# Kernel tuning notes

Measured on AMD Instinct MI355X. Metric: run time of the kernel, lower is better.

Reference implementation:

```python
import jax, jax.numpy as jnp
import numpy as np
import math


def get_slopes(n_heads: int) -> jnp.ndarray:
    """ALiBi head-specific slopes, matching the torch reference."""
    n = 2 ** int(math.floor(math.log2(n_heads)))
    m0 = 2.0 ** (-8.0 / n)
    m = m0 ** jnp.arange(1, n + 1, dtype=jnp.float32)
    if n < n_heads:
        mh0 = 2.0 ** (-4.0 / n)
        mh = mh0 ** jnp.arange(1, 1 + 2 * (n_heads - n), 2, dtype=jnp.float32)
        m = jnp.concatenate([m, mh])
    return m.reshape(1, -1, 1, 1)  # [1, h, 1, 1]


def setup_inputs() -> dict:
    key = jax.random.key(0)
    kq, kk, kv, kb = jax.random.split(key, 4)
    b, h, s_q, s_kv, d = 2, 16, 2048, 2048, 128
    return {
        "query": jax.random.normal(kq, (b, h, s_q, d), dtype=jnp.float32),
        "key": jax.random.normal(kk, (b, h, s_kv, d), dtype=jnp.float32),
        "value": jax.random.normal(kv, (b, h, s_kv, d), dtype=jnp.float32),
        "bias": jax.random.normal(kb, (1, 1, s_q, s_kv), dtype=jnp.float32),
        "is_causal": 1,
        "is_infer": 0,
        "is_alibi": 1,
    }


def reference(query, key, value, bias, is_causal, is_infer, is_alibi):
    _, h, s_q, d = query.shape
    s_kv = key.shape[2]
    attn_scale = 1.0 / math.sqrt(d)

    # S = Q K^T * scale, in fp32 (matches S.to(torch.float32))
    S = jnp.einsum("bhqd,bhkd->bhqk", query, key).astype(jnp.float32) * attn_scale

    if bias is not None:
        S = S + bias

    if is_alibi:
        # relative position (k - q) scaled by per-head slope
        rel = jnp.arange(s_kv, dtype=jnp.float32) - jnp.arange(s_q, dtype=jnp.float32)[:, None]
        S = S + rel * get_slopes(h)

    if is_causal:
        causal_mask = jnp.triu(jnp.ones((s_q, s_kv), dtype=bool), k=1)
        S = jnp.where(causal_mask, -jnp.inf, S)

    Stats = None
    if not is_infer:
        row_max = jnp.max(S, axis=-1, keepdims=True)
        row_sum = jnp.sum(jnp.exp(S - row_max), axis=-1, keepdims=True)
        Stats = row_max + jnp.log(row_sum)  # logsumexp, [b,h,s_q,1]

    P = jax.nn.softmax(S, axis=-1).astype(value.dtype)
    O = jnp.einsum("bhqk,bhkd->bhqd", P, value)
    return (O, Stats)
```

## Files before the change

kernel.cpp:

```cpp
#include <hip/hip_runtime.h>
#include <hip/hip_bf16.h>
#include <math.h>

typedef __bf16 bf16;
typedef __attribute__((ext_vector_type(8))) __bf16 bf16x8;
typedef __attribute__((ext_vector_type(4))) __bf16 bf16x4;
typedef __attribute__((ext_vector_type(4))) float f32x4;
typedef __attribute__((ext_vector_type(16))) float f32x16;
typedef __attribute__((ext_vector_type(4))) unsigned int u32x4;

constexpr int NB = 2, NH = 16, SQ = 2048, SKV = 2048, DH = 128;
constexpr int QB = 128, KVB = 64;
constexpr float SM_SCALE = 0.08838834764831845f;
constexpr float LOG2E = 1.4426950408889634f;
constexpr float DEFER_THR = 7.0f;

#define GLD_LDS(g, l) __builtin_amdgcn_global_load_lds( \
    (const __attribute__((address_space(1))) void*)(g), \
    (__attribute__((address_space(3))) void*)(l), 16, 0, 0)

__device__ __forceinline__ unsigned cvt_pk_bf16(float lo, float hi) {
    unsigned r;
    asm("v_cvt_pk_bf16_f32 %0, %1, %2" : "=v"(r) : "v"(lo), "v"(hi));
    return r;
}
__device__ __forceinline__ void permswap(unsigned &a, unsigned &b) {
    asm("v_permlane32_swap_b32 %0, %1" : "+v"(a), "+v"(b));
}

__global__ __launch_bounds__(256)
void cvt_k_kernel(const float* __restrict__ src, bf16* __restrict__ dst) {
    const size_t i = ((size_t)blockIdx.x * 256 + threadIdx.x) * 8;
    float4 a = *(const float4*)(src + i);
    float4 b = *(const float4*)(src + i + 4);
    bf16x8 f;
    f[0]=(bf16)a.x; f[1]=(bf16)a.y; f[2]=(bf16)a.z; f[3]=(bf16)a.w;
    f[4]=(bf16)b.x; f[5]=(bf16)b.y; f[6]=(bf16)b.z; f[7]=(bf16)b.w;
    *(bf16x8*)(dst + i) = f;
}

__global__ __launch_bounds__(256)
void tr_v_kernel(const float* __restrict__ src, bf16* __restrict__ dst) {
    __shared__ float Tl[64][65];
    const int bh  = blockIdx.y;
    const int kv0 = (int)(blockIdx.x >> 1) * 64;
    const int d0  = (int)(blockIdx.x & 1) * 64;
    const int t   = threadIdx.x;
    const float* sp = src + (size_t)bh * SQ * DH;
#pragma unroll
    for (int i = 0; i < 4; ++i) {
        const int row = i * 16 + (t >> 4);
        const int c4  = (t & 15) * 4;
        *(float4*)&Tl[row][c4] = *(const float4*)(sp + (size_t)(kv0 + row) * DH + d0 + c4);
    }
    __syncthreads();
    bf16* dp = dst + (size_t)bh * DH * SKV;
#pragma unroll
    for (int i = 0; i < 4; ++i) {
        const int d  = i * 16 + (t >> 4);
        const int k4 = (t & 15) * 4;
        bf16x4 o;
        o[0]=(bf16)Tl[k4+0][d]; o[1]=(bf16)Tl[k4+1][d];
        o[2]=(bf16)Tl[k4+2][d]; o[3]=(bf16)Tl[k4+3][d];
        *(bf16x4*)(dp + (size_t)(d0 + d) * SKV + kv0 + k4) = o;
    }
}

__global__ __launch_bounds__(256, 2)
void attn_fwd_kernel(const float* __restrict__ Qg, const bf16* __restrict__ Kb,
                     const bf16* __restrict__ Vb, const float* __restrict__ Bg,
                     float* __restrict__ Og, float* __restrict__ Sg)
{
    __shared__ __attribute__((aligned(16))) bf16 Kl[2][KVB * DH];
    __shared__ __attribute__((aligned(16))) bf16 Vl[2][KVB * DH];

    const int tid = threadIdx.x;
    const int w   = tid >> 6;
    const int ln  = tid & 63;
    const int q5  = ln & 31;
    const int hi  = ln >> 5;
    const int l15 = ln & 15;

    const int bh = blockIdx.x;
    const int h  = bh & (NH - 1);
    const int qt = (blockIdx.y < 8) ? (int)blockIdx.y : 23 - (int)blockIdx.y;
    const int q0 = qt * QB;
    const int qw = q0 + w * 32;
    const int qr = qw + q5;

    const float slope = exp2f(-0.5f * (float)(h + 1));
    const bf16* kbase = Kb + (size_t)bh * SKV * DH;
    const bf16* vbase = Vb + (size_t)bh * DH * SKV;
    const float* bprow = Bg + (size_t)qr * SKV + 4 * hi;

    int ksrc[4], vsrc[4];
#pragma unroll
    for (int i = 0; i < 4; ++i) {
        const int seg = w * 4 + i;
        const int r   = seg * 4 + (ln >> 4);
        const int sl  = l15 ^ (r & 15);
        ksrc[i] = r * DH + (sl << 3);
        vsrc[i] = (2 * r + (sl >> 3)) * SKV + ((sl & 7) << 3);
    }

    auto stage = [&](int kv0n, int buf) {
#pragma unroll
        for (int i = 0; i < 4; ++i)
            GLD_LDS(kbase + (size_t)kv0n * DH + ksrc[i], &Kl[buf][(w * 4 + i) * 512]);
#pragma unroll
        for (int i = 0; i < 4; ++i)
            GLD_LDS(vbase + (size_t)kv0n + vsrc[i], &Vl[buf][(w * 4 + i) * 512]);
    };

    bf16x8 qf[8];
    {
        const float* qrow = Qg + (size_t)bh * SQ * DH + (size_t)qr * DH;
#pragma unroll
        for (int s = 0; s < 8; ++s) {
            const float* qp = qrow + s * 16 + hi * 8;
            float4 a = *(const float4*)qp;
            float4 b = *(const float4*)(qp + 4);
            bf16x8 f;
            f[0]=(bf16)(a.x*SM_SCALE); f[1]=(bf16)(a.y*SM_SCALE);
            f[2]=(bf16)(a.z*SM_SCALE); f[3]=(bf16)(a.w*SM_SCALE);
            f[4]=(bf16)(b.x*SM_SCALE); f[5]=(bf16)(b.y*SM_SCALE);
            f[6]=(bf16)(b.z*SM_SCALE); f[7]=(bf16)(b.w*SM_SCALE);
            qf[s] = f;
        }
    }

    f32x16 acc[4];
#pragma unroll
    for (int dt = 0; dt < 4; ++dt)
#pragma unroll
        for (int e = 0; e < 16; ++e) acc[dt][e] = 0.f;
    float denom = 0.f;
    float mrow = -INFINITY;

    const int ntile = (q0 + QB) / KVB;

    stage(0, 0);
    f32x4 bvf[2][4];
#pragma unroll
    for (int T = 0; T < 2; ++T)
#pragma unroll
        for (int u = 0; u < 4; ++u)
            bvf[T][u] = *(const f32x4*)(bprow + T * 32 + u * 8);
    __syncthreads();
    int cur = 0;

    for (int t = 0; t < ntile; ++t) {
        const int kv0 = t * KVB;
        if (t + 1 < ntile) stage(kv0 + KVB, cur ^ 1);

        const bool liveTile = (kv0 <= qw + 31);
        float p[2][16];
        if (liveTile) {
            f32x16 s0, s1;
#pragma unroll
            for (int e = 0; e < 16; ++e) { s0[e] = 0.f; s1[e] = 0.f; }
            __builtin_amdgcn_s_setprio(1);
#pragma unroll
            for (int s = 0; s < 8; ++s) {
                const int sl = (((2 * s + hi) ^ l15) << 3);
                bf16x8 k0 = *(const bf16x8*)&Kl[cur][q5 * DH + sl];
                bf16x8 k1 = *(const bf16x8*)&Kl[cur][(32 + q5) * DH + sl];
                s0 = __builtin_amdgcn_mfma_f32_32x32x16_bf16(k0, qf[s], s0, 0, 0, 0);
                s1 = __builtin_amdgcn_mfma_f32_32x32x16_bf16(k1, qf[s], s1, 0, 0, 0);
            }
            __builtin_amdgcn_s_setprio(0);

            const int dq2 = qr - kv0 - 4 * hi;
            const float base2 = slope * (float)(-dq2);
            const bool needMask = (kv0 + KVB - 1 > qw);
            if (needMask) {
#pragma unroll
                for (int r = 0; r < 16; ++r) {
                    const int u = r >> 2, v = r & 3;
                    const int k0c = 8 * u + v;
                    const int k1c = 32 + 8 * u + v;
                    float x0 = s0[r] + bvf[0][u][v] + fmaf(slope, (float)k0c, base2);
                    float x1 = s1[r] + bvf[1][u][v] + fmaf(slope, (float)k1c, base2);
                    p[0][r] = (k0c > dq2) ? -INFINITY : x0;
                    p[1][r] = (k1c > dq2) ? -INFINITY : x1;
                }
            } else {
#pragma unroll
                for (int r = 0; r < 16; ++r) {
                    const int u = r >> 2, v = r & 3;
                    p[0][r] = s0[r] + bvf[0][u][v] + fmaf(slope, (float)(8*u+v), base2);
                    p[1][r] = s1[r] + bvf[1][u][v] + fmaf(slope, (float)(32+8*u+v), base2);
                }
            }

            float mt[8];
#pragma unroll
            for (int r = 0; r < 8; ++r)
                mt[r] = fmaxf(fmaxf(p[0][r], p[0][r + 8]), fmaxf(p[1][r], p[1][r + 8]));
            float mx = fmaxf(fmaxf(fmaxf(mt[0], mt[1]), fmaxf(mt[2], mt[3])),
                             fmaxf(fmaxf(mt[4], mt[5]), fmaxf(mt[6], mt[7])));
            mx = fmaxf(mx, __shfl_xor(mx, 32));

            if (__any(mx > mrow + DEFER_THR)) {
                const float mn = fmaxf(mrow, mx);
                const float al = exp2f((mrow - mn) * LOG2E);
                mrow = mn;
#pragma unroll
                for (int dt = 0; dt < 4; ++dt)
#pragma unroll
                    for (int e = 0; e < 16; ++e) acc[dt][e] *= al;
                denom *= al;
            }

#pragma unroll
            for (int T = 0; T < 2; ++T)
#pragma unroll
                for (int r = 0; r < 16; ++r)
                    p[T][r] = exp2f((p[T][r] - mrow) * LOG2E);

            float st[8];
#pragma unroll
            for (int r = 0; r < 8; ++r)
                st[r] = (p[0][r] + p[0][r + 8]) + (p[1][r] + p[1][r + 8]);
            denom += ((st[0] + st[1]) + (st[2] + st[3])) +
                     ((st[4] + st[5]) + (st[6] + st[7]));
        }

        if (t + 1 < ntile) {
#pragma unroll
            for (int T = 0; T < 2; ++T)
#pragma unroll
                for (int u = 0; u < 4; ++u)
                    bvf[T][u] = *(const f32x4*)(bprow + (kv0 + KVB) + T * 32 + u * 8);
        }

        if (liveTile) {
            __builtin_amdgcn_s_setprio(1);
#pragma unroll
            for (int s2 = 0; s2 < 4; ++s2) {
                const int T  = s2 >> 1;
                const int r0 = (s2 & 1) * 8;
                unsigned x1 = cvt_pk_bf16(p[T][r0 + 0], p[T][r0 + 1]);
                unsigned x2 = cvt_pk_bf16(p[T][r0 + 2], p[T][r0 + 3]);
                unsigned y1 = cvt_pk_bf16(p[T][r0 + 4], p[T][r0 + 5]);
                unsigned y2 = cvt_pk_bf16(p[T][r0 + 6], p[T][r0 + 7]);
                permswap(x1, y1);
                permswap(x2, y2);
                u32x4 pw; pw[0] = x1; pw[1] = x2; pw[2] = y1; pw[3] = y2;
                const bf16x8 pb = __builtin_bit_cast(bf16x8, pw);
                const int vsl = (((((q5 & 1) << 3) | (2 * s2 + hi)) ^ (q5 >> 1)) << 3);
#pragma unroll
                for (int dt = 0; dt < 4; ++dt) {
                    bf16x8 vb = *(const bf16x8*)&Vl[cur][(dt * 16 + (q5 >> 1)) * DH + vsl];
                    acc[dt] = __builtin_amdgcn_mfma_f32_32x32x16_bf16(vb, pb, acc[dt], 0, 0, 0);
                }
            }
            __builtin_amdgcn_s_setprio(0);
        }

        __syncthreads();
        cur ^= 1;
    }

    {
        const float dtot = denom + __shfl_xor(denom, 32);
        const float inv = 1.0f / dtot;
        float* orow = Og + (size_t)bh * SQ * DH + (size_t)qr * DH;
#pragma unroll
        for (int dt = 0; dt < 4; ++dt)
#pragma unroll
            for (int u = 0; u < 4; ++u) {
                f32x4 o;
                o[0] = acc[dt][4 * u + 0] * inv;
                o[1] = acc[dt][4 * u + 1] * inv;
                o[2] = acc[dt][4 * u + 2] * inv;
                o[3] = acc[dt][4 * u + 3] * inv;
                *(f32x4*)(orow + dt * 32 + u * 8 + hi * 4) = o;
            }
        if (hi == 0)
            Sg[(size_t)bh * SQ + qr] = mrow + logf(dtot);
    }
}

extern "C" void kernel_launch(void* const* d_in, const int* in_sizes, int n_in,
                              void* d_out, int out_size, void* d_ws, size_t ws_size,
                              hipStream_t stream) {
    const float* Q = (const float*)d_in[0];
    const float* K = (const float*)d_in[1];
    const float* V = (const float*)d_in[2];
    const float* B = (const float*)d_in[3];
    float* O     = (float*)d_out;
    float* Stats = O + (size_t)NB * NH * SQ * DH;

    const size_t nkv = (size_t)NB * NH * SKV * DH;
    bf16* Kb = (bf16*)d_ws;
    bf16* Vt = Kb + nkv;

    cvt_k_kernel<<<(int)(nkv / (256 * 8)), 256, 0, stream>>>(K, Kb);
    tr_v_kernel<<<dim3(64, NB * NH), 256, 0, stream>>>(V, Vt);

    dim3 grid(NB * NH, SQ / QB);
    attn_fwd_kernel<<<grid, 256, 0, stream>>>(Q, Kb, Vt, B, O, Stats);
}
```

Measured before the change: 121.1 us.

## Halve KV tile to 32 rows and raise occupancy to four blocks per CU

Shrinks the KV tile from 64 to 32 keys, halving the LDS double buffers, the score registers and the bias prefetch registers. This allows a launch bound of 4 blocks per CU instead of 2. The V staging layout and swizzled LDS read addresses are reworked to match the narrower tile. The goal is to hide latency through higher occupancy, at the cost of twice as many tile iterations and barriers, plus more per-tile softmax rescale overhead.

```diff
diff --git a/kernel.cpp b/kernel.cpp
--- a/kernel.cpp
+++ b/kernel.cpp
@@ -10,7 +10,7 @@
 typedef __attribute__((ext_vector_type(4))) unsigned int u32x4;
 
 constexpr int NB = 2, NH = 16, SQ = 2048, SKV = 2048, DH = 128;
-constexpr int QB = 128, KVB = 64;
+constexpr int QB = 128, KVB = 32;
 constexpr float SM_SCALE = 0.08838834764831845f;
 constexpr float LOG2E = 1.4426950408889634f;
 constexpr float DEFER_THR = 7.0f;
@@ -66,7 +66,7 @@
     }
 }
 
-__global__ __launch_bounds__(256, 2)
+__global__ __launch_bounds__(256, 4)
 void attn_fwd_kernel(const float* __restrict__ Qg, const bf16* __restrict__ Kb,
                      const bf16* __restrict__ Vb, const float* __restrict__ Bg,
                      float* __restrict__ Og, float* __restrict__ Sg)
@@ -93,23 +93,23 @@
     const bf16* vbase = Vb + (size_t)bh * DH * SKV;
     const float* bprow = Bg + (size_t)qr * SKV + 4 * hi;
 
-    int ksrc[4], vsrc[4];
-#pragma unroll
-    for (int i = 0; i < 4; ++i) {
-        const int seg = w * 4 + i;
+    int ksrc[2], vsrc[2];
+#pragma unroll
+    for (int i = 0; i < 2; ++i) {
+        const int seg = w * 2 + i;
         const int r   = seg * 4 + (ln >> 4);
         const int sl  = l15 ^ (r & 15);
         ksrc[i] = r * DH + (sl << 3);
-        vsrc[i] = (2 * r + (sl >> 3)) * SKV + ((sl & 7) << 3);
+        vsrc[i] = (4 * r + (sl >> 2)) * SKV + ((sl & 3) << 3);
     }
 
     auto stage = [&](int kv0n, int buf) {
 #pragma unroll
-        for (int i = 0; i < 4; ++i)
-            GLD_LDS(kbase + (size_t)kv0n * DH + ksrc[i], &Kl[buf][(w * 4 + i) * 512]);
-#pragma unroll
-        for (int i = 0; i < 4; ++i)
-            GLD_LDS(vbase + (size_t)kv0n + vsrc[i], &Vl[buf][(w * 4 + i) * 512]);
+        for (int i = 0; i < 2; ++i)
+            GLD_LDS(kbase + (size_t)kv0n * DH + ksrc[i], &Kl[buf][(w * 2 + i) * 512]);
+#pragma unroll
+        for (int i = 0; i < 2; ++i)
+            GLD_LDS(vbase + (size_t)kv0n + vsrc[i], &Vl[buf][(w * 2 + i) * 512]);
     };
 
     bf16x8 qf[8];
@@ -140,12 +140,10 @@
     const int ntile = (q0 + QB) / KVB;
 
     stage(0, 0);
-    f32x4 bvf[2][4];
-#pragma unroll
-    for (int T = 0; T < 2; ++T)
-#pragma unroll
-        for (int u = 0; u < 4; ++u)
-            bvf[T][u] = *(const f32x4*)(bprow + T * 32 + u * 8);
+    f32x4 bvf[4];
+#pragma unroll
+    for (int u = 0; u < 4; ++u)
+        bvf[u] = *(const f32x4*)(bprow + u * 8);
     __syncthreads();
     int cur = 0;
 
@@ -154,19 +152,17 @@
         if (t + 1 < ntile) stage(kv0 + KVB, cur ^ 1);
 
         const bool liveTile = (kv0 <= qw + 31);
-        float p[2][16];
+        float p[16];
         if (liveTile) {
-            f32x16 s0, s1;
-#pragma unroll
-            for (int e = 0; e < 16; ++e) { s0[e] = 0.f; s1[e] = 0.f; }
+            f32x16 s0;
+#pragma unroll
+            for (int e = 0; e < 16; ++e) s0[e] = 0.f;
             __builtin_amdgcn_s_setprio(1);
 #pragma unroll
             for (int s = 0; s < 8; ++s) {
                 const int sl = (((2 * s + hi) ^ l15) << 3);
                 bf16x8 k0 = *(const bf16x8*)&Kl[cur][q5 * DH + sl];
-                bf16x8 k1 = *(const bf16x8*)&Kl[cur][(32 + q5) * DH + sl];
                 s0 = __builtin_amdgcn_mfma_f32_32x32x16_bf16(k0, qf[s], s0, 0, 0, 0);
-                s1 = __builtin_amdgcn_mfma_f32_32x32x16_bf16(k1, qf[s], s1, 0, 0, 0);
             }
             __builtin_amdgcn_s_setprio(0);
 
@@ -177,28 +173,23 @@
 #pragma unroll
                 for (int r = 0; r < 16; ++r) {
                     const int u = r >> 2, v = r & 3;
-                    const int k0c = 8 * u + v;
-                    const int k1c = 32 + 8 * u + v;
-                    float x0 = s0[r] + bvf[0][u][v] + fmaf(slope, (float)k0c, base2);
-                    float x1 = s1[r] + bvf[1][u][v] + fmaf(slope, (float)k1c, base2);
-                    p[0][r] = (k0c > dq2) ? -INFINITY : x0;
-                    p[1][r] = (k1c > dq2) ? -INFINITY : x1;
+                    const int koff = 8 * u + v;
+                    float x = s0[r] + bvf[u][v] + fmaf(slope, (float)koff, base2);
+                    p[r] = (koff > dq2) ? -INFINITY : x;
                 }
             } else {
 #pragma unroll
                 for (int r = 0; r < 16; ++r) {
                     const int u = r >> 2, v = r & 3;
-                    p[0][r] = s0[r] + bvf[0][u][v] + fmaf(slope, (float)(8*u+v), base2);
-                    p[1][r] = s1[r] + bvf[1][u][v] + fmaf(slope, (float)(32+8*u+v), base2);
+                    p[r] = s0[r] + bvf[u][v] + fmaf(slope, (float)(8 * u + v), base2);
                 }
             }
 
-            float mt[8];
-#pragma unroll
-            for (int r = 0; r < 8; ++r)
-                mt[r] = fmaxf(fmaxf(p[0][r], p[0][r + 8]), fmaxf(p[1][r], p[1][r + 8]));
-            float mx = fmaxf(fmaxf(fmaxf(mt[0], mt[1]), fmaxf(mt[2], mt[3])),
-                             fmaxf(fmaxf(mt[4], mt[5]), fmaxf(mt[6], mt[7])));
+            float mt[4];
+#pragma unroll
+            for (int r = 0; r < 4; ++r)
+                mt[r] = fmaxf(fmaxf(p[r], p[r + 4]), fmaxf(p[r + 8], p[r + 12]));
+            float mx = fmaxf(fmaxf(mt[0], mt[1]), fmaxf(mt[2], mt[3]));
             mx = fmaxf(mx, __shfl_xor(mx, 32));
 
             if (__any(mx > mrow + DEFER_THR)) {
@@ -213,45 +204,40 @@
             }
 
 #pragma unroll
-            for (int T = 0; T < 2; ++T)
-#pragma unroll
-                for (int r = 0; r < 16; ++r)
-                    p[T][r] = exp2f((p[T][r] - mrow) * LOG2E);
-
-            float st[8];
-#pragma unroll
-            for (int r = 0; r < 8; ++r)
-                st[r] = (p[0][r] + p[0][r + 8]) + (p[1][r] + p[1][r + 8]);
-            denom += ((st[0] + st[1]) + (st[2] + st[3])) +
-                     ((st[4] + st[5]) + (st[6] + st[7]));
+            for (int r = 0; r < 16; ++r)
+                p[r] = exp2f((p[r] - mrow) * LOG2E);
+
+            float st[4];
+#pragma unroll
+            for (int r = 0; r < 4; ++r)
+                st[r] = (p[r] + p[r + 4]) + (p[r + 8] + p[r + 12]);
+            denom += (st[0] + st[1]) + (st[2] + st[3]);
         }
 
         if (t + 1 < ntile) {
 #pragma unroll
-            for (int T = 0; T < 2; ++T)
-#pragma unroll
-                for (int u = 0; u < 4; ++u)
-                    bvf[T][u] = *(const f32x4*)(bprow + (kv0 + KVB) + T * 32 + u * 8);
+            for (int u = 0; u < 4; ++u)
+                bvf[u] = *(const f32x4*)(bprow + (kv0 + KVB) + u * 8);
         }
 
         if (liveTile) {
             __builtin_amdgcn_s_setprio(1);
 #pragma unroll
-            for (int s2 = 0; s2 < 4; ++s2) {
-                const int T  = s2 >> 1;
-                const int r0 = (s2 & 1) * 8;
-                unsigned x1 = cvt_pk_bf16(p[T][r0 + 0], p[T][r0 + 1]);
-                unsigned x2 = cvt_pk_bf16(p[T][r0 + 2], p[T][r0 + 3]);
-                unsigned y1 = cvt_pk_bf16(p[T][r0 + 4], p[T][r0 + 5]);
-                unsigned y2 = cvt_pk_bf16(p[T][r0 + 6], p[T][r0 + 7]);
+            for (int s2 = 0; s2 < 2; ++s2) {
+                const int r0 = s2 * 8;
+                unsigned x1 = cvt_pk_bf16(p[r0 + 0], p[r0 + 1]);
+                unsigned x2 = cvt_pk_bf16(p[r0 + 2], p[r0 + 3]);
+                unsigned y1 = cvt_pk_bf16(p[r0 + 4], p[r0 + 5]);
+                unsigned y2 = cvt_pk_bf16(p[r0 + 6], p[r0 + 7]);
                 permswap(x1, y1);
                 permswap(x2, y2);
                 u32x4 pw; pw[0] = x1; pw[1] = x2; pw[2] = y1; pw[3] = y2;
                 const bf16x8 pb = __builtin_bit_cast(bf16x8, pw);
-                const int vsl = (((((q5 & 1) << 3) | (2 * s2 + hi)) ^ (q5 >> 1)) << 3);
 #pragma unroll
                 for (int dt = 0; dt < 4; ++dt) {
-                    bf16x8 vb = *(const bf16x8*)&Vl[cur][(dt * 16 + (q5 >> 1)) * DH + vsl];
+                    const int vr  = dt * 8 + (q5 >> 2);
+                    const int vsl = ((((q5 & 3) << 2) | (2 * s2 + hi)) ^ (vr & 15)) << 3;
+                    bf16x8 vb = *(const bf16x8*)&Vl[cur][vr * DH + vsl];
                     acc[dt] = __builtin_amdgcn_mfma_f32_32x32x16_bf16(vb, pb, acc[dt], 0, 0, 0);
                 }
             }
```

New measurement: 357.8 us. 2.95x slower.
